# Optimization experiments

Measured on AMD Instinct MI355X. Metric: run time of the kernel, lower is better.

The kernel has to match this reference:

```python
import jax, jax.numpy as jnp
import numpy as np

NUM_THRESH = 1000


def setup_inputs() -> dict:
    key = jax.random.key(0)
    k1, k2 = jax.random.split(key)
    B, C, H, W = 16, 4, 512, 512
    inp = jax.random.uniform(k1, (B, C, H, W), dtype=jnp.float32)
    targ = (jax.random.uniform(k2, (B, C, H, W)) < 0.3).astype(jnp.float32)
    return {"input": inp, "target": targ}


def _max_f1_loss(input, target):
    # input, target: [B, C, H, W]; loss = mean_c (1 - max_t F1_c(t))
    B, C, H, W = input.shape
    N = B * H * W
    x = jnp.transpose(input, (1, 0, 2, 3)).reshape(C, N)   # [C, N]
    y = jnp.transpose(target, (1, 0, 2, 3)).reshape(C, N)  # [C, N]
    thresholds = jnp.linspace(0.0, 1.0, NUM_THRESH).astype(jnp.float32)

    def per_class(xc, yc):
        # idx[n] = number of thresholds strictly below xc[n]  (in [0, 1000])
        # sample n is predicted positive (xc > t_k) exactly for k < idx[n]
        idx = jnp.searchsorted(thresholds, xc, side='left')
        s_y = jax.ops.segment_sum(yc, idx, num_segments=NUM_THRESH + 1)
        s_1 = jax.ops.segment_sum(jnp.ones_like(yc), idx, num_segments=NUM_THRESH + 1)
        cum_y = jnp.cumsum(s_y)[:NUM_THRESH]  # sum of y over samples with idx <= k
        cum_1 = jnp.cumsum(s_1)[:NUM_THRESH]
        total_y = jnp.sum(yc)
        TP = total_y - cum_y            # sum(target * pred) per threshold
        PP = jnp.float32(N) - cum_1     # sum(pred) per threshold
        FP = PP - TP                    # sum((1-target) * pred)
        FN = total_y - TP               # sum(target * (1-pred))
        denom = TP + (FN + FP) * 0.5
        F1 = jnp.where(denom == 0, 0.0, TP / jnp.where(denom == 0, 1.0, denom))
        return 1.0 - jnp.max(F1)

    losses = jax.vmap(per_class)(x, y)  # [C]
    return jnp.mean(losses)


def reference(input, target):
    return _max_f1_loss(input, target)
```

## Files before the change

kernel.cpp:

```cpp
#include <hip/hip_runtime.h>

#define NBINS 1001
#define HIST_BLOCK 256
#define VPT 8
#define ELEMS_PER_BLOCK (HIST_BLOCK * VPT * 4)

typedef float fvec4 __attribute__((ext_vector_type(4)));

__device__ __forceinline__ int bin_of(float v) {
    int k = (int)ceilf(v * 999.0f);
    k = (k < 0) ? 0 : k;
    k = (k > 1000) ? 1000 : k;
    return k;
}

__global__ __launch_bounds__(HIST_BLOCK) void hist_kernel(
    const float* __restrict__ x, const float* __restrict__ y,
    unsigned long long* __restrict__ ghist, int HW)
{
    __shared__ unsigned int lh[NBINS];
    const int tid = threadIdx.x;

    const long long start = (long long)blockIdx.x * ELEMS_PER_BLOCK;
    const int c = (int)((start / HW) & 3);

    const fvec4* __restrict__ x4 = (const fvec4*)(x + start);
    const fvec4* __restrict__ y4 = (const fvec4*)(y + start);

    fvec4 xv[VPT], yv[VPT];
    #pragma unroll
    for (int k = 0; k < VPT; ++k) {
        const int idx = k * HIST_BLOCK + tid;
        xv[k] = __builtin_nontemporal_load(&x4[idx]);
        yv[k] = __builtin_nontemporal_load(&y4[idx]);
    }

    for (int i = tid; i < NBINS; i += HIST_BLOCK) lh[i] = 0u;
    __syncthreads();

    #pragma unroll
    for (int k = 0; k < VPT; ++k) {
        atomicAdd(&lh[bin_of(xv[k].x)], 1u + ((__float_as_uint(yv[k].x) >> 8) & 0x10000u));
        atomicAdd(&lh[bin_of(xv[k].y)], 1u + ((__float_as_uint(yv[k].y) >> 8) & 0x10000u));
        atomicAdd(&lh[bin_of(xv[k].z)], 1u + ((__float_as_uint(yv[k].z) >> 8) & 0x10000u));
        atomicAdd(&lh[bin_of(xv[k].w)], 1u + ((__float_as_uint(yv[k].w) >> 8) & 0x10000u));
    }
    __syncthreads();

    for (int i = tid; i < NBINS; i += HIST_BLOCK) {
        unsigned int v = lh[i];
        if (v) {
            unsigned long long add = (unsigned long long)(v & 0xffffu)
                                   | ((unsigned long long)(v >> 16) << 32);
            atomicAdd(&ghist[(size_t)c * NBINS + i], add);
        }
    }
}

__global__ __launch_bounds__(1024) void f1_kernel(
    const unsigned long long* __restrict__ ghist, float* __restrict__ out)
{
    __shared__ unsigned long long wtot[4][16];
    __shared__ float wmax[4][16];
    const int tid  = threadIdx.x;
    const int lane = tid & 63;
    const int wave = tid >> 6;

    unsigned long long v[4];
    #pragma unroll
    for (int c = 0; c < 4; ++c)
        v[c] = (tid < NBINS) ? ghist[(size_t)c * NBINS + tid] : 0ULL;

    #pragma unroll
    for (int off = 1; off < 64; off <<= 1) {
        #pragma unroll
        for (int c = 0; c < 4; ++c) {
            unsigned long long t = __shfl_up(v[c], off, 64);
            if (lane >= off) v[c] += t;
        }
    }
    if (lane == 63) {
        #pragma unroll
        for (int c = 0; c < 4; ++c) wtot[c][wave] = v[c];
    }
    __syncthreads();

    if (wave == 0) {
        const int c = lane >> 4, w = lane & 15;
        unsigned long long t = wtot[c][w];
        #pragma unroll
        for (int off = 1; off < 16; off <<= 1) {
            unsigned long long s = __shfl_up(t, off, 16);
            if (w >= off) t += s;
        }
        wtot[c][w] = t;
    }
    __syncthreads();

    float m[4];
    #pragma unroll
    for (int c = 0; c < 4; ++c) {
        unsigned long long cum = v[c];
        if (wave > 0) cum += wtot[c][wave - 1];
        unsigned long long tot = wtot[c][15];
        unsigned int total_cnt = (unsigned int)(tot & 0xffffffffULL);
        unsigned int total_y   = (unsigned int)(tot >> 32);
        float f1 = 0.0f;
        if (tid < NBINS - 1) {
            unsigned int cnt_cum = (unsigned int)(cum & 0xffffffffULL);
            unsigned int y_cum   = (unsigned int)(cum >> 32);
            unsigned int TP = total_y - y_cum;
            unsigned int PP = total_cnt - cnt_cum;
            unsigned int denom = total_y + PP;
            f1 = (denom == 0u) ? 0.0f : (2.0f * (float)TP) / (float)denom;
        }
        m[c] = f1;
    }

    #pragma unroll
    for (int off = 32; off > 0; off >>= 1) {
        #pragma unroll
        for (int c = 0; c < 4; ++c)
            m[c] = fmaxf(m[c], __shfl_down(m[c], off, 64));
    }
    if (lane == 0) {
        #pragma unroll
        for (int c = 0; c < 4; ++c) wmax[c][wave] = m[c];
    }
    __syncthreads();

    if (tid == 0) {
        float loss = 0.0f;
        #pragma unroll
        for (int c = 0; c < 4; ++c) {
            float mm = wmax[c][0];
            #pragma unroll
            for (int w = 1; w < 16; ++w) mm = fmaxf(mm, wmax[c][w]);
            loss += 1.0f - mm;
        }
        out[0] = loss * 0.25f;
    }
}

extern "C" void kernel_launch(void* const* d_in, const int* in_sizes, int n_in,
                              void* d_out, int out_size, void* d_ws, size_t ws_size,
                              hipStream_t stream) {
    const float* x = (const float*)d_in[0];
    const float* y = (const float*)d_in[1];
    float* out = (float*)d_out;

    const int H = 512, W = 512;
    const int HW = H * W;
    const long long total = (long long)in_sizes[0];

    unsigned long long* ghist = (unsigned long long*)d_ws;

    (void)hipMemsetAsync(d_ws, 0, (size_t)4 * NBINS * sizeof(unsigned long long), stream);

    const int nblocks = (int)(total / ELEMS_PER_BLOCK);
    hist_kernel<<<nblocks, HIST_BLOCK, 0, stream>>>(x, y, ghist, HW);
    f1_kernel<<<1, 1024, 0, stream>>>(ghist, out);
    (void)n_in; (void)out_size; (void)ws_size;
}
```

Baseline: 147.3 us.

## Fuse F1 scan into histogram kernel via last-block-done counter

Removes the separate single-block F1 kernel launch. Each histogram block bumps a global completion counter after its global atomics, and the last block to finish loads the histograms and does the prefix scan and max-F1 reduction. Because that block has 256 threads, each thread handles 4 bins and the 4 classes are processed in sequence. This saves one kernel launch and its gap, at the cost of a serial tail inside the last block plus extra fences.

Measured after the change: 246.8 us. 1.68x slower.

```diff
diff --git a/kernel.cpp b/kernel.cpp
--- a/kernel.cpp
+++ b/kernel.cpp
@@ -14,9 +14,9 @@
     return k;
 }
 
-__global__ __launch_bounds__(HIST_BLOCK) void hist_kernel(
+__global__ __launch_bounds__(HIST_BLOCK) void hist_f1_kernel(
     const float* __restrict__ x, const float* __restrict__ y,
-    unsigned long long* __restrict__ ghist, int HW)
+    unsigned long long* __restrict__ ghist, float* __restrict__ out, int HW)
 {
     __shared__ unsigned int lh[NBINS];
     const int tid = threadIdx.x;
@@ -55,91 +55,82 @@
             atomicAdd(&ghist[(size_t)c * NBINS + i], add);
         }
     }
-}
 
-__global__ __launch_bounds__(1024) void f1_kernel(
-    const unsigned long long* __restrict__ ghist, float* __restrict__ out)
-{
-    __shared__ unsigned long long wtot[4][16];
-    __shared__ float wmax[4][16];
-    const int tid  = threadIdx.x;
+    __syncthreads();
+    __shared__ unsigned long long s_done;
+    if (tid == 0) {
+        __threadfence();
+        s_done = atomicAdd(&ghist[(size_t)4 * NBINS], 1ULL);
+    }
+    __syncthreads();
+    if (s_done != (unsigned long long)(gridDim.x - 1)) return;
+
+    __threadfence();
+    __shared__ unsigned long long wscan[4];
+    __shared__ float wmax[4];
     const int lane = tid & 63;
     const int wave = tid >> 6;
 
-    unsigned long long v[4];
-    #pragma unroll
-    for (int c = 0; c < 4; ++c)
-        v[c] = (tid < NBINS) ? ghist[(size_t)c * NBINS + tid] : 0ULL;
+    float loss = 0.0f;
+    for (int cc = 0; cc < 4; ++cc) {
+        unsigned long long inc[4];
+        unsigned long long run = 0;
+        #pragma unroll
+        for (int j = 0; j < 4; ++j) {
+            const int bin = 4 * tid + j;
+            unsigned long long b = 0;
+            if (bin < NBINS)
+                b = __hip_atomic_load(&ghist[(size_t)cc * NBINS + bin],
+                                      __ATOMIC_RELAXED, __HIP_MEMORY_SCOPE_AGENT);
+            run += b;
+            inc[j] = run;
+        }
+        const unsigned long long tsum = run;
 
-    #pragma unroll
-    for (int off = 1; off < 64; off <<= 1) {
+        unsigned long long sc = tsum;
         #pragma unroll
-        for (int c = 0; c < 4; ++c) {
-            unsigned long long t = __shfl_up(v[c], off, 64);
-            if (lane >= off) v[c] += t;
+        for (int off = 1; off < 64; off <<= 1) {
+            unsigned long long t = __shfl_up(sc, off, 64);
+            if (lane >= off) sc += t;
         }
+        if (lane == 63) wscan[wave] = sc;
+        __syncthreads();
+
+        unsigned long long woff = 0;
+        #pragma unroll
+        for (int w = 0; w < 4; ++w)
+            if (w < wave) woff += wscan[w];
+        const unsigned long long tot = wscan[0] + wscan[1] + wscan[2] + wscan[3];
+        const unsigned long long base = woff + sc - tsum;
+
+        const unsigned int total_cnt = (unsigned int)(tot & 0xffffffffULL);
+        const unsigned int total_y   = (unsigned int)(tot >> 32);
+
+        float m = 0.0f;
+        #pragma unroll
+        for (int j = 0; j < 4; ++j) {
+            const int bin = 4 * tid + j;
+            if (bin < NBINS - 1) {
+                const unsigned long long cum = base + inc[j];
+                const unsigned int cnt_cum = (unsigned int)(cum & 0xffffffffULL);
+                const unsigned int y_cum   = (unsigned int)(cum >> 32);
+                const unsigned int TP = total_y - y_cum;
+                const unsigned int PP = total_cnt - cnt_cum;
+                const unsigned int denom = total_y + PP;
+                const float f1 = (denom == 0u) ? 0.0f : (2.0f * (float)TP) / (float)denom;
+                m = fmaxf(m, f1);
+            }
+        }
+        #pragma unroll
+        for (int off = 32; off > 0; off >>= 1)
+            m = fmaxf(m, __shfl_down(m, off, 64));
+        if (lane == 0) wmax[wave] = m;
+        __syncthreads();
+        if (tid == 0)
+            loss += 1.0f - fmaxf(fmaxf(wmax[0], wmax[1]), fmaxf(wmax[2], wmax[3]));
+        __syncthreads();
     }
-    if (lane == 63) {
-        #pragma unroll
-        for (int c = 0; c < 4; ++c) wtot[c][wave] = v[c];
-    }
-    __syncthreads();
-
-    if (wave == 0) {
-        const int c = lane >> 4, w = lane & 15;
-        unsigned long long t = wtot[c][w];
-        #pragma unroll
-        for (int off = 1; off < 16; off <<= 1) {
-            unsigned long long s = __shfl_up(t, off, 16);
-            if (w >= off) t += s;
-        }
-        wtot[c][w] = t;
-    }
-    __syncthreads();
-
-    float m[4];
-    #pragma unroll
-    for (int c = 0; c < 4; ++c) {
-        unsigned long long cum = v[c];
-        if (wave > 0) cum += wtot[c][wave - 1];
-        unsigned long long tot = wtot[c][15];
-        unsigned int total_cnt = (unsigned int)(tot & 0xffffffffULL);
-        unsigned int total_y   = (unsigned int)(tot >> 32);
-        float f1 = 0.0f;
-        if (tid < NBINS - 1) {
-            unsigned int cnt_cum = (unsigned int)(cum & 0xffffffffULL);
-            unsigned int y_cum   = (unsigned int)(cum >> 32);
-            unsigned int TP = total_y - y_cum;
-            unsigned int PP = total_cnt - cnt_cum;
-            unsigned int denom = total_y + PP;
-            f1 = (denom == 0u) ? 0.0f : (2.0f * (float)TP) / (float)denom;
-        }
-        m[c] = f1;
-    }
-
-    #pragma unroll
-    for (int off = 32; off > 0; off >>= 1) {
-        #pragma unroll
-        for (int c = 0; c < 4; ++c)
-            m[c] = fmaxf(m[c], __shfl_down(m[c], off, 64));
-    }
-    if (lane == 0) {
-        #pragma unroll
-        for (int c = 0; c < 4; ++c) wmax[c][wave] = m[c];
-    }
-    __syncthreads();
-
-    if (tid == 0) {
-        float loss = 0.0f;
-        #pragma unroll
-        for (int c = 0; c < 4; ++c) {
-            float mm = wmax[c][0];
-            #pragma unroll
-            for (int w = 1; w < 16; ++w) mm = fmaxf(mm, wmax[c][w]);
-            loss += 1.0f - mm;
-        }
-        out[0] = loss * 0.25f;
-    }
+    if (tid == 0) out[0] = loss * 0.25f;
 }
 
 extern "C" void kernel_launch(void* const* d_in, const int* in_sizes, int n_in,
@@ -155,10 +146,9 @@
 
     unsigned long long* ghist = (unsigned long long*)d_ws;
 
-    (void)hipMemsetAsync(d_ws, 0, (size_t)4 * NBINS * sizeof(unsigned long long), stream);
+    (void)hipMemsetAsync(d_ws, 0, (size_t)(4 * NBINS + 1) * sizeof(unsigned long long), stream);
 
     const int nblocks = (int)(total / ELEMS_PER_BLOCK);
-    hist_kernel<<<nblocks, HIST_BLOCK, 0, stream>>>(x, y, ghist, HW);
-    f1_kernel<<<1, 1024, 0, stream>>>(ghist, out);
+    hist_f1_kernel<<<nblocks, HIST_BLOCK, 0, stream>>>(x, y, ghist, out, HW);
     (void)n_in; (void)out_size; (void)ws_size;
 }
```
